# Kernel optimization log

Measured on AMD Instinct MI355X. Metric: run time of the kernel, lower is better.

Reference implementation:

```python
import jax, jax.numpy as jnp
import numpy as np

NEG_SLOPE = 0.2
HEADS = 4
C = 64            # hidden_channels
NUM_CLASSES = 12
NUM_GRAPHS = 512


def gatv2_conv(x, src, dst, Wl, Wr, att, bias, heads, out_ch, num_nodes):
    """PyG GATv2Conv: gather -> LeakyReLU attention -> segment softmax -> scatter.
    x: [N, Fin]; src/dst: [E]; Wl/Wr: [Fin, heads*out_ch]; att: [heads, out_ch]; bias: [heads*out_ch].
    Messages flow src -> dst; heads are concatenated."""
    xl = (x @ Wl).reshape(num_nodes, heads, out_ch)  # source-side transform
    xr = (x @ Wr).reshape(num_nodes, heads, out_ch)  # target-side transform
    e = jax.nn.leaky_relu(xl[src] + xr[dst], NEG_SLOPE)      # [E, H, C]
    score = jnp.einsum('ehc,hc->eh', e, att)                  # [E, H]
    smax = jax.ops.segment_max(score, dst, num_segments=num_nodes)  # [N, H]
    ex = jnp.exp(score - smax[dst])
    denom = jax.ops.segment_sum(ex, dst, num_segments=num_nodes)    # [N, H]
    alpha = ex / (denom[dst] + 1e-16)                         # [E, H]
    out = jax.ops.segment_sum(alpha[:, :, None] * xl[src], dst, num_segments=num_nodes)
    return out.reshape(num_nodes, heads * out_ch) + bias


def add_self_loops(edge_index, num_nodes):
    loop = jnp.arange(num_nodes, dtype=edge_index.dtype)
    src = jnp.concatenate([edge_index[0], loop])
    dst = jnp.concatenate([edge_index[1], loop])
    return src, dst


def setup_inputs() -> dict:
    key = jax.random.key(0)
    ks = jax.random.split(key, 20)
    N, F, E = 50000, 128, 800000

    def w(k, shape):
        return (jax.random.normal(k, shape) * 0.1).astype(jnp.float32)

    inp = {
        'x': jax.random.normal(ks[0], (N, F), dtype=jnp.float32),
        'edge_index': jax.random.randint(ks[1], (2, E), 0, N),
        'batch': jnp.sort(jax.random.randint(ks[2], (N,), 0, NUM_GRAPHS)),
        # conv1: (-1,-1) lazy -> Fin=F, heads=4
        'W1l': w(ks[3], (F, HEADS * C)), 'W1r': w(ks[4], (F, HEADS * C)),
        'a1': w(ks[5], (HEADS, C)), 'b1': jnp.zeros((HEADS * C,), jnp.float32),
        # conv2: Fin = hidden*heads = 256, heads=4
        'W2l': w(ks[6], (HEADS * C, HEADS * C)), 'W2r': w(ks[7], (HEADS * C, HEADS * C)),
        'a2': w(ks[8], (HEADS, C)), 'b2': jnp.zeros((HEADS * C,), jnp.float32),
        # conv3: Fin = 256, heads=1
        'W3l': w(ks[9], (HEADS * C, C)), 'W3r': w(ks[10], (HEADS * C, C)),
        'a3': w(ks[11], (1, C)), 'b3': jnp.zeros((C,), jnp.float32),
        # MLP head (lazy Linear(-1, ...) resolves to C after conv3 heads=1)
        'lin1_w': w(ks[12], (C, C)), 'lin1_b': jnp.zeros((C,), jnp.float32),
        'lin2_w': w(ks[13], (C, C)), 'lin2_b': jnp.zeros((C,), jnp.float32),
        'lin3_w': w(ks[14], (C, NUM_CLASSES)), 'lin3_b': jnp.zeros((NUM_CLASSES,), jnp.float32),
    }
    return inp


def reference(x, edge_index, batch,
              W1l, W1r, a1, b1,
              W2l, W2r, a2, b2,
              W3l, W3r, a3, b3,
              lin1_w, lin1_b, lin2_w, lin2_b, lin3_w, lin3_b):
    N = x.shape[0]
    src0, dst0 = edge_index[0], edge_index[1]          # conv1: add_self_loops=False
    src1, dst1 = add_self_loops(edge_index, N)         # conv2/3: add_self_loops=True

    h = gatv2_conv(x, src0, dst0, W1l, W1r, a1, b1, HEADS, C, N)
    h = jax.nn.relu(h)
    h = gatv2_conv(h, src1, dst1, W2l, W2r, a2, b2, HEADS, C, N)
    h = jax.nn.relu(h)
    h = gatv2_conv(h, src1, dst1, W3l, W3r, a3, b3, 1, C, N)

    # global mean pool over graphs
    s = jax.ops.segment_sum(h, batch, num_segments=NUM_GRAPHS)
    cnt = jax.ops.segment_sum(jnp.ones((N, 1), h.dtype), batch, num_segments=NUM_GRAPHS)
    g = s / jnp.maximum(cnt, 1.0)

    g = jax.nn.relu(g @ lin1_w + lin1_b)
    # dropout p=0.5 is identity in eval mode
    g = jax.nn.relu(g @ lin2_w + lin2_b)
    return jax.nn.softmax(g @ lin3_w + lin3_b, axis=1)
```

## Files before the change

### kernel.cpp

```cpp
#include <hip/hip_runtime.h>
#include <hip/hip_bf16.h>
#include <cstdint>
#include <cstddef>

typedef short bf16x8 __attribute__((ext_vector_type(8)));
typedef float f32x4 __attribute__((ext_vector_type(4)));
typedef unsigned short u16x4v __attribute__((ext_vector_type(4)));

__device__ __forceinline__ float bf2f(unsigned short u) {
  union { unsigned int u; float f; } v; v.u = ((unsigned int)u) << 16; return v.f;
}
__device__ __forceinline__ unsigned short f2bf(float f) {
  union { float f; unsigned int u; } v; v.f = f;
  unsigned int r = v.u + 0x7fffu + ((v.u >> 16) & 1u);
  return (unsigned short)(r >> 16);
}
__device__ __forceinline__ void gll16(const void* g, void* l) {
  __builtin_amdgcn_global_load_lds(
      (const __attribute__((address_space(1))) unsigned int*)g,
      (__attribute__((address_space(3))) unsigned int*)l, 16, 0, 0);
}
template<int CTRL>
__device__ __forceinline__ float dpp_ror_add(float p) {
  int t = __builtin_amdgcn_update_dpp(0, __builtin_bit_cast(int, p), CTRL, 0xf, 0xf, true);
  return p + __builtin_bit_cast(float, t);
}
__device__ __forceinline__ float row16_sum(float p) {
  p = dpp_ror_add<0x121>(p);
  p = dpp_ror_add<0x122>(p);
  p = dpp_ror_add<0x124>(p);
  p = dpp_ror_add<0x128>(p);
  return p;
}

#define LOG2E 1.44269504088896f
#define THR2  11.5415603271f

struct WPack {
  const float* in[6];
  unsigned short* out[6];
  int K[6], Ncol[6];
  int start[7];
};
__global__ __launch_bounds__(256) void convert_all(WPack p) {
  int idx = blockIdx.x * 256 + threadIdx.x;
  #pragma unroll
  for (int s = 0; s < 6; ++s) {
    if (idx >= p.start[s] && idx < p.start[s + 1]) {
      int lidx = idx - p.start[s];
      int k = lidx / p.Ncol[s], n = lidx % p.Ncol[s];
      p.out[s][n * p.K[s] + k] = f2bf(p.in[s][lidx]);
    }
  }
}

__global__ __launch_bounds__(256) void convert_x(const float* __restrict__ in,
                                                 unsigned short* __restrict__ out, int n4) {
  int i = blockIdx.x * 256 + threadIdx.x;
  if (i < n4) {
    f32x4 v = *reinterpret_cast<const f32x4*>(in + (size_t)i * 4);
    u16x4v o;
    #pragma unroll
    for (int j = 0; j < 4; ++j) o[j] = f2bf(v[j]);
    *reinterpret_cast<u16x4v*>(out + (size_t)i * 4) = o;
  }
}

template<int BN, int WAVES_M, int WAVES_N>
__global__ __launch_bounds__(256) void gemm_dual(
    const unsigned short* __restrict__ A,
    const unsigned short* __restrict__ BtL, const unsigned short* __restrict__ BtR,
    unsigned short* __restrict__ outL, unsigned short* __restrict__ outR,
    int M, int K, int Ncol) {
  constexpr int BM = 128, BK = 64;
  constexpr int WTM = BM / WAVES_M, WTN = BN / WAVES_N;
  constexpr int MR = WTM / 16, NR = WTN / 16;
  const unsigned short* __restrict__ Bt = blockIdx.z ? BtR : BtL;
  unsigned short* __restrict__ outp = blockIdx.z ? outR : outL;

  __shared__ alignas(16) unsigned short lAt[BM * BK];
  __shared__ alignas(16) unsigned short lBt[BN * BK];

  int t = threadIdx.x;
  int lane = t & 63, wid = t >> 6;
  int wm = wid / WAVES_N, wn = wid % WAVES_N;
  int rowBase = blockIdx.x * BM;
  int colBase = blockIdx.y * BN;

  f32x4 acc[MR][NR] = {};

  for (int k0 = 0; k0 < K; k0 += BK) {
    #pragma unroll
    for (int p = 0; p < BM / 32; ++p) {
      int chunk = wid * (BM / 32) + p;
      int row = chunk * 8 + (lane >> 3);
      int c = (lane & 7) ^ (row & 7);
      gll16(A + (size_t)(rowBase + row) * K + k0 + c * 8, &lAt[chunk * 512]);
    }
    #pragma unroll
    for (int p = 0; p < BN / 32; ++p) {
      int chunk = wid * (BN / 32) + p;
      int row = chunk * 8 + (lane >> 3);
      int c = (lane & 7) ^ (row & 7);
      gll16(Bt + (size_t)(colBase + row) * K + k0 + c * 8, &lBt[chunk * 512]);
    }
    __syncthreads();
    #pragma unroll
    for (int kk = 0; kk < 2; ++kk) {
      bf16x8 af[MR], bfr[NR];
      int cidx = kk * 4 + (lane >> 4);
      #pragma unroll
      for (int mi = 0; mi < MR; ++mi) {
        int row = wm * WTM + mi * 16 + (lane & 15);
        af[mi] = *reinterpret_cast<const bf16x8*>(&lAt[row * 64 + ((cidx ^ (row & 7)) * 8)]);
      }
      #pragma unroll
      for (int ni = 0; ni < NR; ++ni) {
        int row = wn * WTN + ni * 16 + (lane & 15);
        bfr[ni] = *reinterpret_cast<const bf16x8*>(&lBt[row * 64 + ((cidx ^ (row & 7)) * 8)]);
      }
      #pragma unroll
      for (int mi = 0; mi < MR; ++mi)
        #pragma unroll
        for (int ni = 0; ni < NR; ++ni)
          acc[mi][ni] = __builtin_amdgcn_mfma_f32_16x16x32_bf16(af[mi], bfr[ni], acc[mi][ni], 0, 0, 0);
    }
    __syncthreads();
  }
  #pragma unroll
  for (int mi = 0; mi < MR; ++mi)
    #pragma unroll
    for (int ni = 0; ni < NR; ++ni) {
      int col = colBase + wn * WTN + ni * 16 + (lane & 15);
      #pragma unroll
      for (int r = 0; r < 4; ++r) {
        int row = rowBase + wm * WTM + mi * 16 + (lane >> 4) * 4 + r;
        if (row < M) outp[(size_t)row * Ncol + col] = f2bf(acc[mi][ni][r]);
      }
    }
}

__global__ __launch_bounds__(256) void hist_kernel(const int* __restrict__ dst, int* __restrict__ counts, int E) {
  int e = blockIdx.x * 256 + threadIdx.x;
  if (e < E) atomicAdd(&counts[dst[e]], 1);
}

__global__ __launch_bounds__(256) void scan_block_deg(
    const int* __restrict__ in, int* __restrict__ out, int* __restrict__ sums,
    int* __restrict__ binTotal, int* __restrict__ blockBase, int n) {
  __shared__ int lh[256];
  __shared__ int wsum[4];
  lh[threadIdx.x] = 0;
  __syncthreads();
  int i = blockIdx.x * 256 + threadIdx.x;
  int lane = threadIdx.x & 63, wid = threadIdx.x >> 6;
  int v = (i < n) ? in[i] : 0;
  if (i < n) atomicAdd(&lh[v < 255 ? v : 255], 1);
  int s = v;
  #pragma unroll
  for (int d = 1; d < 64; d <<= 1) { int tt = __shfl_up(s, d); if (lane >= d) s += tt; }
  if (lane == 63) wsum[wid] = s;
  __syncthreads();
  int off = 0;
  for (int w = 0; w < wid; ++w) off += wsum[w];
  if (i < n) out[i] = off + s - v;
  if (threadIdx.x == 255) sums[blockIdx.x] = off + s;
  int c = lh[threadIdx.x];
  blockBase[blockIdx.x * 256 + threadIdx.x] = c ? atomicAdd(&binTotal[threadIdx.x], c) : 0;
}

__global__ __launch_bounds__(256) void scan2_offsets(
    const int* __restrict__ bsums, int* __restrict__ boffs,
    const int* __restrict__ binTotal, int* __restrict__ binStart, int n) {
  __shared__ int ws[4];
  int t = threadIdx.x;
  int lane = t & 63, w = t >> 6;
  {
    int v = (t < n) ? bsums[t] : 0;
    int s = v;
    #pragma unroll
    for (int d = 1; d < 64; d <<= 1) { int tt = __shfl_up(s, d); if (lane >= d) s += tt; }
    if (lane == 63) ws[w] = s;
    __syncthreads();
    int off = 0;
    for (int u = 0; u < w; ++u) off += ws[u];
    if (t < n) boffs[t] = off + s - v;
    __syncthreads();
  }
  {
    int v = binTotal[255 - t];
    int s = v;
    #pragma unroll
    for (int d = 1; d < 64; d <<= 1) { int tt = __shfl_up(s, d); if (lane >= d) s += tt; }
    if (lane == 63) ws[w] = s;
    __syncthreads();
    int off = 0;
    for (int u = 0; u < w; ++u) off += ws[u];
    binStart[255 - t] = off + s - v;
  }
}

__global__ __launch_bounds__(256) void scan_add_place(
    int* __restrict__ rs, const int* __restrict__ boffs, int* __restrict__ cursor,
    const int* __restrict__ counts, const int* __restrict__ binStart,
    const int* __restrict__ blockBase, int* __restrict__ perm, int n, int E) {
  __shared__ int lcur[256];
  lcur[threadIdx.x] = binStart[threadIdx.x] + blockBase[blockIdx.x * 256 + threadIdx.x];
  __syncthreads();
  int i = blockIdx.x * 256 + threadIdx.x;
  if (i < n) {
    int v = rs[i] + boffs[blockIdx.x];
    rs[i] = v;
    cursor[i] = v;
    int d = counts[i]; if (d > 255) d = 255;
    perm[atomicAdd(&lcur[d], 1)] = i;
  }
  if (i == 0) rs[n] = E;
}

__global__ __launch_bounds__(256) void scatter_kernel(const int* __restrict__ src, const int* __restrict__ dst,
                                                      int* __restrict__ cursor, int* __restrict__ csr, int E) {
  int e = blockIdx.x * 256 + threadIdx.x;
  if (e < E) {
    int p = atomicAdd(&cursor[dst[e]], 1);
    csr[p] = src[e];
  }
}

template<bool SELF, bool RELU>
__global__ __launch_bounds__(256) void edge_agg4(
    const unsigned short* __restrict__ xl, const unsigned short* __restrict__ xr,
    const float* __restrict__ att, const float* __restrict__ bias,
    const int* __restrict__ rowstart, const int* __restrict__ csr,
    const int* __restrict__ perm,
    unsigned short* __restrict__ out, int N) {
  int wave = threadIdx.x >> 6, lane = threadIdx.x & 63;
  int gid = blockIdx.x * 4 + wave;
  if (gid >= N) return;
  int node = perm[gid];

  float attv[4];
  {
    f32x4 a4 = *reinterpret_cast<const f32x4*>(att + lane * 4);
    #pragma unroll
    for (int j = 0; j < 4; ++j) attv[j] = a4[j] * LOG2E;
  }
  float xrv[4];
  {
    u16x4v r4 = *reinterpret_cast<const u16x4v*>(xr + (size_t)node * 256 + lane * 4);
    #pragma unroll
    for (int j = 0; j < 4; ++j) xrv[j] = bf2f(r4[j]);
  }

  int s0 = rowstart[node], s1 = rowstart[node + 1];
  int end = s1 + (SELF ? 1 : 0);

  auto score4 = [&](const float* xv) -> float {
    float t0 = xv[0] + xrv[0]; t0 = fmaxf(t0, 0.2f * t0);
    float t1 = xv[1] + xrv[1]; t1 = fmaxf(t1, 0.2f * t1);
    float t2 = xv[2] + xrv[2]; t2 = fmaxf(t2, 0.2f * t2);
    float t3 = xv[3] + xrv[3]; t3 = fmaxf(t3, 0.2f * t3);
    float pa = t0 * attv[0];
    float pb = t1 * attv[1];
    pa = fmaf(t2, attv[2], pa);
    pb = fmaf(t3, attv[3], pb);
    return row16_sum(pa + pb);
  };
  auto loadx = [&](int s, float* xv) {
    u16x4v r = *reinterpret_cast<const u16x4v*>(xl + (size_t)s * 256 + lane * 4);
    #pragma unroll
    for (int j = 0; j < 4; ++j) xv[j] = bf2f(r[j]);
  };

  float m = 0.f, l = 0.f;
  float acc[4] = {0.f, 0.f, 0.f, 0.f};

  int i = s0;
  if (i < end) {
    int s = (i < s1) ? csr[i] : node;
    float xv[4];
    loadx(s, xv);
    m = score4(xv);
    l = 1.f;
    #pragma unroll
    for (int j = 0; j < 4; ++j) acc[j] = xv[j];
    ++i;
  }
  for (; i + 4 <= end; i += 4) {
    int iu = __builtin_amdgcn_readfirstlane(i);
    int s_[4];
    float x_[4][4], p_[4], w_[4];
    #pragma unroll
    for (int q = 0; q < 4; ++q) s_[q] = (iu + q < s1) ? csr[iu + q] : node;
    #pragma unroll
    for (int q = 0; q < 4; ++q) loadx(s_[q], x_[q]);
    #pragma unroll
    for (int q = 0; q < 4; ++q) p_[q] = score4(x_[q]);
    float mx = fmaxf(fmaxf(p_[0], p_[1]), fmaxf(p_[2], p_[3]));
    if (__any(mx > m + THR2)) {
      float mn = fmaxf(m, mx);
      float sc = __builtin_amdgcn_exp2f(m - mn);
      l *= sc;
      #pragma unroll
      for (int j = 0; j < 4; ++j) acc[j] *= sc;
      m = mn;
    }
    #pragma unroll
    for (int q = 0; q < 4; ++q) w_[q] = __builtin_amdgcn_exp2f(p_[q] - m);
    l += (w_[0] + w_[1]) + (w_[2] + w_[3]);
    #pragma unroll
    for (int j = 0; j < 4; ++j)
      acc[j] = fmaf(w_[0], x_[0][j],
               fmaf(w_[1], x_[1][j],
               fmaf(w_[2], x_[2][j],
               fmaf(w_[3], x_[3][j], acc[j]))));
  }
  for (; i < end; ++i) {
    int s = (i < s1) ? csr[i] : node;
    float xv[4];
    loadx(s, xv);
    float p = score4(xv);
    if (__any(p > m + THR2)) {
      float mn = fmaxf(m, p);
      float sc = __builtin_amdgcn_exp2f(m - mn);
      l *= sc;
      #pragma unroll
      for (int j = 0; j < 4; ++j) acc[j] *= sc;
      m = mn;
    }
    float w = __builtin_amdgcn_exp2f(p - m);
    l += w;
    #pragma unroll
    for (int j = 0; j < 4; ++j) acc[j] = fmaf(w, xv[j], acc[j]);
  }

  float rec = 1.f / (l + 1e-16f);
  f32x4 b4 = *reinterpret_cast<const f32x4*>(bias + lane * 4);
  u16x4v w4;
  #pragma unroll
  for (int j = 0; j < 4; ++j) {
    float o = fmaf(acc[j], rec, b4[j]);
    if (RELU) o = fmaxf(o, 0.f);
    w4[j] = f2bf(o);
  }
  *reinterpret_cast<u16x4v*>(out + (size_t)node * 256 + lane * 4) = w4;
}

template<bool SELF, bool RELU>
__global__ __launch_bounds__(256) void edge_agg1(
    const unsigned short* __restrict__ xl, const unsigned short* __restrict__ xr,
    const float* __restrict__ att, const float* __restrict__ bias,
    const int* __restrict__ rowstart, const int* __restrict__ csr,
    const int* __restrict__ perm,
    unsigned short* __restrict__ out, int N) {
  int wave = threadIdx.x >> 6, lane = threadIdx.x & 63;
  int gid = blockIdx.x * 4 + wave;
  if (gid >= N) return;
  int node = perm[gid];

  float attv = att[lane] * LOG2E;
  float xrv = bf2f(xr[(size_t)node * 64 + lane]);

  int s0 = rowstart[node], s1 = rowstart[node + 1];
  int end = s1 + (SELF ? 1 : 0);

  auto score = [&](float xv) {
    float tv = xv + xrv;
    tv = fmaxf(tv, 0.2f * tv);
    float p = row16_sum(tv * attv);
    p += __shfl_xor(p, 16);
    p += __shfl_xor(p, 32);
    return p;
  };

  float m = 0.f, l = 0.f, acc = 0.f;

  int i = s0;
  if (i < end) {
    int s = (i < s1) ? csr[i] : node;
    float xv = bf2f(xl[(size_t)s * 64 + lane]);
    m = score(xv);
    l = 1.f;
    acc = xv;
    ++i;
  }
  for (; i + 4 <= end; i += 4) {
    int iu = __builtin_amdgcn_readfirstlane(i);
    int s_[4];
    float x_[4], p_[4], w_[4];
    #pragma unroll
    for (int q = 0; q < 4; ++q) s_[q] = (iu + q < s1) ? csr[iu + q] : node;
    #pragma unroll
    for (int q = 0; q < 4; ++q) x_[q] = bf2f(xl[(size_t)s_[q] * 64 + lane]);
    #pragma unroll
    for (int q = 0; q < 4; ++q) p_[q] = score(x_[q]);
    float mx = fmaxf(fmaxf(p_[0], p_[1]), fmaxf(p_[2], p_[3]));
    if (__any(mx > m + THR2)) {
      float mn = fmaxf(m, mx);
      float sc = __builtin_amdgcn_exp2f(m - mn);
      l *= sc; acc *= sc; m = mn;
    }
    #pragma unroll
    for (int q = 0; q < 4; ++q) w_[q] = __builtin_amdgcn_exp2f(p_[q] - m);
    l += (w_[0] + w_[1]) + (w_[2] + w_[3]);
    acc = fmaf(w_[0], x_[0], fmaf(w_[1], x_[1], fmaf(w_[2], x_[2], fmaf(w_[3], x_[3], acc))));
  }
  for (; i < end; ++i) {
    int s = (i < s1) ? csr[i] : node;
    float xv = bf2f(xl[(size_t)s * 64 + lane]);
    float p = score(xv);
    if (__any(p > m + THR2)) {
      float mn = fmaxf(m, p);
      float sc = __builtin_amdgcn_exp2f(m - mn);
      l *= sc; acc *= sc; m = mn;
    }
    float w = __builtin_amdgcn_exp2f(p - m);
    l += w;
    acc = fmaf(w, xv, acc);
  }

  float rec = 1.f / (l + 1e-16f);
  float o = fmaf(acc, rec, bias[lane]);
  if (RELU) o = fmaxf(o, 0.f);
  out[(size_t)node * 64 + lane] = f2bf(o);
}

__global__ __launch_bounds__(256) void pool_mlp(
    const unsigned short* __restrict__ h, const int* __restrict__ batch,
    const float* __restrict__ w1, const float* __restrict__ b1,
    const float* __restrict__ w2, const float* __restrict__ b2,
    const float* __restrict__ w3, const float* __restrict__ b3,
    float* __restrict__ out, int N) {
  int g = blockIdx.x;
  int lo = 0, hi = N;
  while (lo < hi) { int mid = (lo + hi) >> 1; if (batch[mid] < g) lo = mid + 1; else hi = mid; }
  int n0 = lo;
  hi = N;
  while (lo < hi) { int mid = (lo + hi) >> 1; if (batch[mid] < g + 1) lo = mid + 1; else hi = mid; }
  int n1 = lo;

  int t = threadIdx.x;
  int c2 = t & 31, r = t >> 5;
  float ax = 0.f, ay = 0.f;
  for (int n = n0 + r; n < n1; n += 8) {
    unsigned int u = *reinterpret_cast<const unsigned int*>(h + (size_t)n * 64 + c2 * 2);
    ax += bf2f((unsigned short)(u & 0xffffu));
    ay += bf2f((unsigned short)(u >> 16));
  }
  __shared__ float redx[8][32], redy[8][32];
  __shared__ float sh[64];
  redx[r][c2] = ax; redy[r][c2] = ay;
  __syncthreads();
  if (t < 64) {
    int lane = t;
    float s = 0.f;
    #pragma unroll
    for (int q = 0; q < 8; ++q) s += (lane & 1) ? redy[q][lane >> 1] : redx[q][lane >> 1];
    float cnt = fmaxf((float)(n1 - n0), 1.f);
    sh[lane] = s / cnt;
    float h1 = b1[lane];
    for (int k = 0; k < 64; ++k) h1 = fmaf(sh[k], w1[k * 64 + lane], h1);
    h1 = fmaxf(h1, 0.f);
    sh[lane] = h1;
    float h2 = b2[lane];
    for (int k = 0; k < 64; ++k) h2 = fmaf(sh[k], w2[k * 64 + lane], h2);
    h2 = fmaxf(h2, 0.f);
    sh[lane] = h2;
    float lg = -INFINITY;
    if (lane < 12) {
      lg = b3[lane];
      for (int k = 0; k < 64; ++k) lg = fmaf(sh[k], w3[k * 12 + lane], lg);
    }
    float mx = lg;
    #pragma unroll
    for (int msk = 1; msk < 64; msk <<= 1) mx = fmaxf(mx, __shfl_xor(mx, msk));
    float ex = (lane < 12) ? __expf(lg - mx) : 0.f;
    float sm = ex;
    #pragma unroll
    for (int msk = 1; msk < 64; msk <<= 1) sm += __shfl_xor(sm, msk);
    if (lane < 12) out[(size_t)g * 12 + lane] = ex / sm;
  }
}

extern "C" void kernel_launch(void* const* d_in, const int* in_sizes, int n_in,
                              void* d_out, int out_size, void* d_ws, size_t ws_size,
                              hipStream_t stream) {
  const float* x    = (const float*)d_in[0];
  const int* edge   = (const int*)d_in[1];
  const int* batch  = (const int*)d_in[2];
  const float* W1l  = (const float*)d_in[3];
  const float* W1r  = (const float*)d_in[4];
  const float* a1   = (const float*)d_in[5];
  const float* b1   = (const float*)d_in[6];
  const float* W2l  = (const float*)d_in[7];
  const float* W2r  = (const float*)d_in[8];
  const float* a2   = (const float*)d_in[9];
  const float* b2   = (const float*)d_in[10];
  const float* W3l  = (const float*)d_in[11];
  const float* W3r  = (const float*)d_in[12];
  const float* a3   = (const float*)d_in[13];
  const float* b3   = (const float*)d_in[14];
  const float* lw1  = (const float*)d_in[15];
  const float* lb1  = (const float*)d_in[16];
  const float* lw2  = (const float*)d_in[17];
  const float* lb2  = (const float*)d_in[18];
  const float* lw3  = (const float*)d_in[19];
  const float* lb3  = (const float*)d_in[20];

  const int E = in_sizes[1] / 2;
  const int N = in_sizes[2];
  const int F0 = in_sizes[0] / N;
  const int G = out_size / 12;
  const int* src = edge;
  const int* dst = edge + E;

  const int gx = (N + 127) / 128;
  const int Mpad = gx * 128;
  const int nb = (N + 255) / 256;

  char* p = (char*)d_ws;
  auto alloc = [&](size_t bytes) { char* q = p; p += (bytes + 255) & ~(size_t)255; return q; };
  unsigned short* bufA = (unsigned short*)alloc((size_t)Mpad * 256 * 2);
  unsigned short* bufB = (unsigned short*)alloc((size_t)Mpad * 256 * 2);
  unsigned short* bufH = (unsigned short*)alloc((size_t)Mpad * 256 * 2);
  unsigned short* xbf  = (unsigned short*)alloc((size_t)Mpad * 128 * 2);
  unsigned short* Wt1L = (unsigned short*)alloc(128 * 256 * 2);
  unsigned short* Wt1R = (unsigned short*)alloc(128 * 256 * 2);
  unsigned short* Wt2L = (unsigned short*)alloc(256 * 256 * 2);
  unsigned short* Wt2R = (unsigned short*)alloc(256 * 256 * 2);
  unsigned short* Wt3L = (unsigned short*)alloc(256 * 64 * 2);
  unsigned short* Wt3R = (unsigned short*)alloc(256 * 64 * 2);
  int* counts    = (int*)alloc((size_t)N * 4);
  int* binTotal  = (int*)alloc(256 * 4);
  int* binStart  = (int*)alloc(256 * 4);
  int* blockBase = (int*)alloc((size_t)nb * 256 * 4);
  int* rowstart  = (int*)alloc((size_t)(N + 1) * 4);
  int* cursor    = (int*)alloc((size_t)N * 4);
  int* perm      = (int*)alloc((size_t)N * 4);
  int* bsums     = (int*)alloc(4096 * 4);
  int* boffs     = (int*)alloc(4096 * 4);
  int* csr       = (int*)alloc((size_t)E * 4);

  size_t countsPad = ((size_t)N * 4 + 255) & ~(size_t)255;
  hipMemsetAsync(counts, 0, countsPad + 256 * 4, stream);
  hist_kernel<<<(E + 255) / 256, 256, 0, stream>>>(dst, counts, E);
  scan_block_deg<<<nb, 256, 0, stream>>>(counts, rowstart, bsums, binTotal, blockBase, N);
  scan2_offsets<<<1, 256, 0, stream>>>(bsums, boffs, binTotal, binStart, nb);
  scan_add_place<<<nb, 256, 0, stream>>>(rowstart, boffs, cursor, counts, binStart, blockBase, perm, N, E);
  scatter_kernel<<<(E + 255) / 256, 256, 0, stream>>>(src, dst, cursor, csr, E);

  {
    WPack wp;
    const float* ins[6] = {W1l, W1r, W2l, W2r, W3l, W3r};
    unsigned short* outs[6] = {Wt1L, Wt1R, Wt2L, Wt2R, Wt3L, Wt3R};
    int Ks[6] = {F0, F0, 256, 256, 256, 256};
    int Ns[6] = {256, 256, 256, 256, 64, 64};
    int acc0 = 0;
    for (int s = 0; s < 6; ++s) {
      wp.in[s] = ins[s]; wp.out[s] = outs[s]; wp.K[s] = Ks[s]; wp.Ncol[s] = Ns[s];
      wp.start[s] = acc0; acc0 += Ks[s] * Ns[s];
    }
    wp.start[6] = acc0;
    convert_all<<<(acc0 + 255) / 256, 256, 0, stream>>>(wp);
  }
  {
    int n4 = (N * F0) / 4;
    convert_x<<<(n4 + 255) / 256, 256, 0, stream>>>(x, xbf, n4);
  }

  int ne = (N + 3) / 4;

  gemm_dual<128, 2, 2><<<dim3(gx, 2, 2), 256, 0, stream>>>(xbf, Wt1L, Wt1R, bufA, bufB, N, F0, 256);
  edge_agg4<false, true><<<ne, 256, 0, stream>>>(bufA, bufB, a1, b1, rowstart, csr, perm, bufH, N);

  gemm_dual<128, 2, 2><<<dim3(gx, 2, 2), 256, 0, stream>>>(bufH, Wt2L, Wt2R, bufA, bufB, N, 256, 256);
  edge_agg4<true, true><<<ne, 256, 0, stream>>>(bufA, bufB, a2, b2, rowstart, csr, perm, bufH, N);

  gemm_dual<64, 4, 1><<<dim3(gx, 1, 2), 256, 0, stream>>>(bufH, Wt3L, Wt3R, bufA, bufB, N, 256, 64);
  edge_agg1<true, false><<<ne, 256, 0, stream>>>(bufA, bufB, a3, b3, rowstart, csr, perm, bufH, N);

  pool_mlp<<<G, 256, 0, stream>>>(bufH, batch, lw1, lb1, lw2, lb2, lw3, lb3,
                                  (float*)d_out, N);
}
```

Measured before the change: 460.8 us.

## Concatenate left/right weights into one GEMM with wider 512-thread tiles

New measurement: 447.2 us. 1.03x faster.

```diff
diff --git a/kernel.cpp b/kernel.cpp
--- a/kernel.cpp
+++ b/kernel.cpp
@@ -66,17 +66,18 @@
   }
 }
 
-template<int BN, int WAVES_M, int WAVES_N>
-__global__ __launch_bounds__(256) void gemm_dual(
+template<int BN, int NL>
+__global__ __launch_bounds__(512) void gemm_cat(
     const unsigned short* __restrict__ A,
-    const unsigned short* __restrict__ BtL, const unsigned short* __restrict__ BtR,
+    const unsigned short* __restrict__ Wt,
     unsigned short* __restrict__ outL, unsigned short* __restrict__ outR,
-    int M, int K, int Ncol) {
+    int M, int K) {
   constexpr int BM = 128, BK = 64;
-  constexpr int WTM = BM / WAVES_M, WTN = BN / WAVES_N;
-  constexpr int MR = WTM / 16, NR = WTN / 16;
-  const unsigned short* __restrict__ Bt = blockIdx.z ? BtR : BtL;
-  unsigned short* __restrict__ outp = blockIdx.z ? outR : outL;
+  constexpr int WAVES_M = 2, WAVES_N = 4;
+  constexpr int WTM = BM / WAVES_M;
+  constexpr int WTN = BN / WAVES_N;
+  constexpr int MR = WTM / 16;
+  constexpr int NR = WTN / 16;
 
   __shared__ alignas(16) unsigned short lAt[BM * BK];
   __shared__ alignas(16) unsigned short lBt[BN * BK];
@@ -91,18 +92,18 @@
 
   for (int k0 = 0; k0 < K; k0 += BK) {
     #pragma unroll
-    for (int p = 0; p < BM / 32; ++p) {
-      int chunk = wid * (BM / 32) + p;
+    for (int p = 0; p < BM / 64; ++p) {
+      int chunk = wid * (BM / 64) + p;
       int row = chunk * 8 + (lane >> 3);
       int c = (lane & 7) ^ (row & 7);
       gll16(A + (size_t)(rowBase + row) * K + k0 + c * 8, &lAt[chunk * 512]);
     }
     #pragma unroll
-    for (int p = 0; p < BN / 32; ++p) {
-      int chunk = wid * (BN / 32) + p;
+    for (int p = 0; p < BN / 64; ++p) {
+      int chunk = wid * (BN / 64) + p;
       int row = chunk * 8 + (lane >> 3);
       int c = (lane & 7) ^ (row & 7);
-      gll16(Bt + (size_t)(colBase + row) * K + k0 + c * 8, &lBt[chunk * 512]);
+      gll16(Wt + (size_t)(colBase + row) * K + k0 + c * 8, &lBt[chunk * 512]);
     }
     __syncthreads();
     #pragma unroll
@@ -132,10 +133,11 @@
     #pragma unroll
     for (int ni = 0; ni < NR; ++ni) {
       int col = colBase + wn * WTN + ni * 16 + (lane & 15);
+      unsigned short* op = (col < NL) ? (outL + col) : (outR + (col - NL));
       #pragma unroll
       for (int r = 0; r < 4; ++r) {
         int row = rowBase + wm * WTM + mi * 16 + (lane >> 4) * 4 + r;
-        if (row < M) outp[(size_t)row * Ncol + col] = f2bf(acc[mi][ni][r]);
+        if (row < M) op[(size_t)row * NL] = f2bf(acc[mi][ni][r]);
       }
     }
 }
@@ -524,12 +526,9 @@
   unsigned short* bufB = (unsigned short*)alloc((size_t)Mpad * 256 * 2);
   unsigned short* bufH = (unsigned short*)alloc((size_t)Mpad * 256 * 2);
   unsigned short* xbf  = (unsigned short*)alloc((size_t)Mpad * 128 * 2);
-  unsigned short* Wt1L = (unsigned short*)alloc(128 * 256 * 2);
-  unsigned short* Wt1R = (unsigned short*)alloc(128 * 256 * 2);
-  unsigned short* Wt2L = (unsigned short*)alloc(256 * 256 * 2);
-  unsigned short* Wt2R = (unsigned short*)alloc(256 * 256 * 2);
-  unsigned short* Wt3L = (unsigned short*)alloc(256 * 64 * 2);
-  unsigned short* Wt3R = (unsigned short*)alloc(256 * 64 * 2);
+  unsigned short* Wc1  = (unsigned short*)alloc(512 * 128 * 2);
+  unsigned short* Wc2  = (unsigned short*)alloc(512 * 256 * 2);
+  unsigned short* Wc3  = (unsigned short*)alloc(128 * 256 * 2);
   int* counts    = (int*)alloc((size_t)N * 4);
   int* binTotal  = (int*)alloc(256 * 4);
   int* binStart  = (int*)alloc(256 * 4);
@@ -552,7 +551,7 @@
   {
     WPack wp;
     const float* ins[6] = {W1l, W1r, W2l, W2r, W3l, W3r};
-    unsigned short* outs[6] = {Wt1L, Wt1R, Wt2L, Wt2R, Wt3L, Wt3R};
+    unsigned short* outs[6] = {Wc1, Wc1 + 256 * 128, Wc2, Wc2 + 256 * 256, Wc3, Wc3 + 64 * 256};
     int Ks[6] = {F0, F0, 256, 256, 256, 256};
     int Ns[6] = {256, 256, 256, 256, 64, 64};
     int acc0 = 0;
@@ -570,13 +569,13 @@
 
   int ne = (N + 3) / 4;
 
-  gemm_dual<128, 2, 2><<<dim3(gx, 2, 2), 256, 0, stream>>>(xbf, Wt1L, Wt1R, bufA, bufB, N, F0, 256);
+  gemm_cat<256, 256><<<dim3(gx, 2), 512, 0, stream>>>(xbf, Wc1, bufA, bufB, N, F0);
   edge_agg4<false, true><<<ne, 256, 0, stream>>>(bufA, bufB, a1, b1, rowstart, csr, perm, bufH, N);
 
-  gemm_dual<128, 2, 2><<<dim3(gx, 2, 2), 256, 0, stream>>>(bufH, Wt2L, Wt2R, bufA, bufB, N, 256, 256);
+  gemm_cat<256, 256><<<dim3(gx, 2), 512, 0, stream>>>(bufH, Wc2, bufA, bufB, N, 256);
   edge_agg4<true, true><<<ne, 256, 0, stream>>>(bufA, bufB, a2, b2, rowstart, csr, perm, bufH, N);
 
-  gemm_dual<64, 4, 1><<<dim3(gx, 1, 2), 256, 0, stream>>>(bufH, Wt3L, Wt3R, bufA, bufB, N, 256, 64);
+  gemm_cat<128, 64><<<dim3(gx, 1), 512, 0, stream>>>(bufH, Wc3, bufA, bufB, N, 256);
   edge_agg1<true, false><<<ne, 256, 0, stream>>>(bufA, bufB, a3, b3, rowstart, csr, perm, bufH, N);
 
   pool_mlp<<<G, 256, 0, stream>>>(bufH, batch, lw1, lb1, lw2, lb2, lw3, lb3,
```
